# Optimization experiments

Hardware: AMD Instinct MI355X
Metric: run time of the kernel (lower is better)

Reference implementation:

```python
import jax, jax.numpy as jnp
import numpy as np


def setup_inputs() -> dict:
    key = jax.random.key(0)
    k0, k1, k2, k3, k4 = jax.random.split(key, 5)
    B, W, C, C2, D = 4, 64, 512, 512, 64  # D = C // k, k=8
    x = jax.random.normal(k0, (B, W, W, C), dtype=jnp.float32)
    input_h = jax.random.normal(k1, (B, W, W, C2), dtype=jnp.float32)
    f = jax.random.normal(k2, (1, 1, C2, D), dtype=jnp.float32) * 0.02
    g = jax.random.normal(k3, (1, 1, C, D), dtype=jnp.float32) * 0.02
    gamma = jax.random.uniform(k4, (1,), dtype=jnp.float32)
    return {"x": x, "input_h": input_h, "f": f, "g": g, "gamma": gamma}


def reference(x, input_h, f, g, gamma):
    # x: [B,W,W,C] NHWC, input_h: [B,W,W,C2], f: [1,1,C2,D], g: [1,1,C,D]
    B, W, _, C = x.shape
    C2 = input_h.shape[-1]
    N = W * W
    # 1x1 convs == per-pixel channel matmuls
    f_proj = jnp.einsum('bhwc,cd->bhwd', input_h, f[0, 0])  # [B,W,W,D]
    g_proj = jnp.einsum('bhwc,cd->bhwd', x, g[0, 0])        # [B,W,W,D]
    f_flat = f_proj.reshape(B, N, -1)
    g_flat = g_proj.reshape(B, N, -1)
    # unscaled attention scores over spatial positions
    s = jnp.einsum('bnd,bmd->bnm', g_flat, f_flat)          # [B,N,N]
    beta = jax.nn.softmax(s, axis=-1)
    h_flat = input_h.reshape(B, N, C2)
    o = jnp.einsum('bnm,bmc->bnc', beta, h_flat).reshape(B, W, W, C2)
    # mix_concat == 'mix': learned residual mix
    return gamma * o + x
```

## Files before the change

### kernel.cpp

```cpp
#include <hip/hip_runtime.h>
#include <hip/hip_bf16.h>
#include <cstdint>
#include <cstddef>


#define NPOS 4096
#define CCH  512
#define DQK  64
#define LSTR 72

typedef __attribute__((ext_vector_type(8)))  short s8v;
typedef __attribute__((ext_vector_type(4)))  short s4v;
typedef __attribute__((ext_vector_type(4)))  float f4v;

__device__ __forceinline__ float bf2f(unsigned short u) {
    unsigned int x = ((unsigned int)u) << 16;
    return __builtin_bit_cast(float, x);
}
__device__ __forceinline__ unsigned short f2bf(float f) {
    unsigned int u = __builtin_bit_cast(unsigned int, f);
    u += 0x7fffu + ((u >> 16) & 1u);
    return (unsigned short)(u >> 16);
}

__global__ __launch_bounds__(256) void wt_kernel(
    const float* __restrict__ f, const float* __restrict__ g,
    unsigned short* __restrict__ fT, unsigned short* __restrict__ gT)
{
    int gid = blockIdx.x * 256 + threadIdx.x;
    for (int e = 0; e < 4; ++e) {
        int i = e * 16384 + gid;
        int which = i >> 15;
        int j = i & 32767;
        int d = j >> 9, k = j & 511;
        const float* s = which ? g : f;
        unsigned short* dst = which ? gT : fT;
        dst[j] = f2bf(s[k * 64 + d]);
    }
}

__global__ __launch_bounds__(256) void vt_kernel(
    const float* __restrict__ ih, unsigned short* __restrict__ Vt)
{
    __shared__ unsigned short T[64 * 65];
    const int tid = threadIdx.x;
    const int bidx = blockIdx.x;
    const int bb = bidx >> 9;
    const int rem = bidx & 511;
    const int ct = rem >> 6;
    const int nt = rem & 63;

    for (int p = 0; p < 4; ++p) {
        int idx = p * 256 + tid;
        int r = idx >> 4, gg = idx & 15;
        f4v v = *(const f4v*)(ih + ((size_t)bb * NPOS + nt * 64 + r) * CCH + ct * 64 + gg * 4);
        for (int j = 0; j < 4; ++j) T[r * 65 + gg * 4 + j] = f2bf(v[j]);
    }
    __syncthreads();
    for (int p = 0; p < 2; ++p) {
        int idx = p * 256 + tid;
        int c = idx >> 3, ng = idx & 7;
        unsigned short tmp[8];
        for (int j = 0; j < 8; ++j) tmp[j] = T[(ng * 8 + j) * 65 + c];
        *(s8v*)(Vt + ((size_t)bb * CCH + ct * 64 + c) * NPOS + nt * 64 + ng * 8) = *(const s8v*)tmp;
    }
}

__global__ __launch_bounds__(256) void proj_kernel(
    const float* __restrict__ x,  const float* __restrict__ ih,
    const unsigned short* __restrict__ gT, const unsigned short* __restrict__ fT,
    unsigned short* __restrict__ Qg, unsigned short* __restrict__ Kf)
{
    __shared__ __align__(16) short Alds[128 * LSTR];
    __shared__ __align__(16) short Wlds[64 * LSTR];
    const int tid = threadIdx.x;
    const int wave = tid >> 6, lane = tid & 63;
    const int n15 = lane & 15, quad = lane >> 4;
    const int which = blockIdx.x >> 7;
    const int rb = (blockIdx.x & 127) * 128;
    const float* src = which ? ih : x;
    const unsigned short* wT  = which ? fT : gT;
    unsigned short* dst = which ? Kf : Qg;

    f4v acc[2][4];
    for (int i = 0; i < 2; ++i)
        for (int j = 0; j < 4; ++j)
            acc[i][j] = f4v{0.f, 0.f, 0.f, 0.f};

    for (int kc = 0; kc < 8; ++kc) {
        for (int p = 0; p < 8; ++p) {
            int idx = p * 256 + tid;
            int r = idx >> 4, gg = idx & 15;
            f4v v = *(const f4v*)(src + (size_t)(rb + r) * CCH + kc * 64 + gg * 4);
            s4v tv;
            for (int j = 0; j < 4; ++j) tv[j] = (short)f2bf(v[j]);
            *(s4v*)&Alds[r * LSTR + gg * 4] = tv;
        }
        for (int p = 0; p < 2; ++p) {
            int idx = p * 256 + tid;
            int c = idx >> 3, gg = idx & 7;
            *(s8v*)&Wlds[c * LSTR + gg * 8] =
                *(const s8v*)(wT + (size_t)c * CCH + kc * 64 + gg * 8);
        }
        __syncthreads();
        for (int kk = 0; kk < 2; ++kk) {
            s8v af0 = *(const s8v*)&Alds[(wave * 32 +      n15) * LSTR + kk * 32 + quad * 8];
            s8v af1 = *(const s8v*)&Alds[(wave * 32 + 16 + n15) * LSTR + kk * 32 + quad * 8];
            for (int ct = 0; ct < 4; ++ct) {
                s8v bf = *(const s8v*)&Wlds[(ct * 16 + n15) * LSTR + kk * 32 + quad * 8];
                acc[0][ct] = __builtin_amdgcn_mfma_f32_16x16x32_bf16(af0, bf, acc[0][ct], 0, 0, 0);
                acc[1][ct] = __builtin_amdgcn_mfma_f32_16x16x32_bf16(af1, bf, acc[1][ct], 0, 0, 0);
            }
        }
        __syncthreads();
    }
    for (int rt = 0; rt < 2; ++rt)
        for (int ct = 0; ct < 4; ++ct)
            for (int r = 0; r < 4; ++r) {
                int row = wave * 32 + rt * 16 + quad * 4 + r;
                int col = ct * 16 + n15;
                dst[(size_t)(rb + row) * DQK + col] = f2bf(acc[rt][ct][r]);
            }
}

__global__ __launch_bounds__(512) void flash_kernel(
    const unsigned short* __restrict__ Qg,
    const unsigned short* __restrict__ Kf,
    const unsigned short* __restrict__ Vt,
    const float* __restrict__ xin,
    const float* __restrict__ gptr,
    float* __restrict__ out)
{
    __shared__ __align__(16) short Klds[2 * 64 * LSTR];
    __shared__ __align__(16) short Plds[64 * LSTR];
    __shared__ float l_s[64];

    const int tid = threadIdx.x;
    const int wave = tid >> 6;
    const int lane = tid & 63;
    const int n15 = lane & 15, quad = lane >> 4;
    const int bid = blockIdx.x;
    const int xcd = bid & 7;
    const int b = xcd >> 1;
    const int qt = (xcd & 1) + ((bid >> 3) << 1);
    const int qbase = qt * 64;

    const float SOFT_M = 20.0f;
    float lpart = 0.0f;

    f4v acc[4][4];
    for (int i = 0; i < 4; ++i)
        for (int j = 0; j < 4; ++j)
            acc[i][j] = f4v{0.f, 0.f, 0.f, 0.f};

    const int ti = wave >> 1;
    const int mi0 = (wave & 1) * 2;
    s8v qf[2];
    {
        const unsigned short* qp =
            Qg + ((size_t)b * NPOS + qbase + ti * 16 + n15) * DQK + quad * 8;
        qf[0] = *(const s8v*)(qp);
        qf[1] = *(const s8v*)(qp + 32);
    }

    const int cb = wave * 64;
    const unsigned short* Vb = Vt + (size_t)b * CCH * NPOS;

    const int kr = tid >> 3, kg = tid & 7;
    const unsigned short* kbase_p = Kf + ((size_t)b * NPOS + kr) * DQK + kg * 8;
    s8v kreg = *(const s8v*)(kbase_p);

    for (int kb = 0; kb < NPOS / 64; ++kb) {
        const int m0 = kb * 64;
        *(s8v*)&Klds[(kb & 1) * 64 * LSTR + kr * LSTR + kg * 8] = kreg;
        if (kb + 1 < NPOS / 64)
            kreg = *(const s8v*)(kbase_p + (size_t)(m0 + 64) * DQK);
        s8v vf[4][2];
        for (int ct = 0; ct < 4; ++ct) {
            const unsigned short* vp =
                Vb + (size_t)(cb + ct * 16 + n15) * NPOS + m0 + quad * 8;
            vf[ct][0] = *(const s8v*)(vp);
            vf[ct][1] = *(const s8v*)(vp + 32);
        }
        __syncthreads();

        {
            const short* Kb = &Klds[(kb & 1) * 64 * LSTR];
            for (int mm = 0; mm < 2; ++mm) {
                const int mi = mi0 + mm;
                f4v s4 = f4v{0.f, 0.f, 0.f, 0.f};
                for (int ks = 0; ks < 2; ++ks) {
                    s8v kf = *(const s8v*)&Kb[(mi * 16 + n15) * LSTR + ks * 32 + quad * 8];
                    s4 = __builtin_amdgcn_mfma_f32_16x16x32_bf16(qf[ks], kf, s4, 0, 0, 0);
                }
                const int col = mi * 16 + n15;
                const int row0 = ti * 16 + quad * 4;
                for (int r = 0; r < 4; ++r)
                    Plds[(row0 + r) * LSTR + col] =
                        (short)f2bf(__expf(fminf(s4[r], 80.0f) - SOFT_M));
            }
        }
        __syncthreads();

        {
            const int r = tid >> 3, j8 = tid & 7;
            s8v p8 = *(const s8v*)&Plds[r * LSTR + j8 * 8];
            float ls = 0.f;
            for (int e = 0; e < 8; ++e) ls += bf2f((unsigned short)p8[e]);
            lpart += ls;
        }
        for (int kk = 0; kk < 2; ++kk) {
            s8v af[4];
            for (int q4 = 0; q4 < 4; ++q4)
                af[q4] = *(const s8v*)&Plds[(q4 * 16 + n15) * LSTR + kk * 32 + quad * 8];
            for (int q4 = 0; q4 < 4; ++q4)
                for (int ct = 0; ct < 4; ++ct)
                    acc[q4][ct] = __builtin_amdgcn_mfma_f32_16x16x32_bf16(
                        af[q4], vf[ct][kk], acc[q4][ct], 0, 0, 0);
        }
    }

    lpart += __shfl_xor(lpart, 1);
    lpart += __shfl_xor(lpart, 2);
    lpart += __shfl_xor(lpart, 4);
    if ((tid & 7) == 0) l_s[tid >> 3] = lpart;
    __syncthreads();

    const float gamma = gptr[0];
    for (int q4 = 0; q4 < 4; ++q4) {
        for (int r = 0; r < 4; ++r) {
            const int row = q4 * 16 + quad * 4 + r;
            const float sc = gamma / l_s[row];
            for (int ct = 0; ct < 4; ++ct) {
                const int col = cb + ct * 16 + n15;
                const size_t idx = ((size_t)b * NPOS + qbase + row) * CCH + col;
                out[idx] = acc[q4][ct][r] * sc + xin[idx];
            }
        }
    }
}

extern "C" void kernel_launch(void* const* d_in, const int* in_sizes, int n_in,
                              void* d_out, int out_size, void* d_ws, size_t ws_size,
                              hipStream_t stream)
{
    const float* x     = (const float*)d_in[0];
    const float* ih    = (const float*)d_in[1];
    const float* f     = (const float*)d_in[2];
    const float* g     = (const float*)d_in[3];
    const float* gamma = (const float*)d_in[4];
    float* out = (float*)d_out;

    char* ws = (char*)d_ws;
    unsigned short* fT = (unsigned short*)(ws + 0);
    unsigned short* gT = (unsigned short*)(ws + 65536);
    unsigned short* Qg = (unsigned short*)(ws + 131072);
    unsigned short* Kf = (unsigned short*)(ws + 2228224);
    unsigned short* Vt = (unsigned short*)(ws + 4325376);

    wt_kernel<<<64, 256, 0, stream>>>(f, g, fT, gT);
    vt_kernel<<<2048, 256, 0, stream>>>(ih, Vt);
    proj_kernel<<<256, 256, 0, stream>>>(x, ih, gT, fT, Qg, Kf);
    flash_kernel<<<256, 512, 0, stream>>>(Qg, Kf, Vt, x, gamma, out);
}
```

Before: 279.5 us.

## Split flash attention across channel halves and load K directly into registers

The flash kernel now runs 512 blocks of 256 threads. Each block covers half the output channels, and each wave computes the scores for its own 16 query rows. K is loaded straight from global memory into registers instead of being staged in LDS, and P is double-buffered, which removes one barrier per key tile. Row sums are accumulated in fp32 from the unrounded probabilities. The projection kernel also drops LDS and computes directly from global memory with one wave per 16 rows. The cost is that scores and exponentials are recomputed twice, once per channel half, and global K loads are redundant across waves.

```diff
diff --git a/kernel.cpp b/kernel.cpp
--- a/kernel.cpp
+++ b/kernel.cpp
@@ -10,7 +10,6 @@
 #define LSTR 72
 
 typedef __attribute__((ext_vector_type(8)))  short s8v;
-typedef __attribute__((ext_vector_type(4)))  short s4v;
 typedef __attribute__((ext_vector_type(4)))  float f4v;
 
 __device__ __forceinline__ float bf2f(unsigned short u) {
@@ -71,59 +70,41 @@
     const unsigned short* __restrict__ gT, const unsigned short* __restrict__ fT,
     unsigned short* __restrict__ Qg, unsigned short* __restrict__ Kf)
 {
-    __shared__ __align__(16) short Alds[128 * LSTR];
-    __shared__ __align__(16) short Wlds[64 * LSTR];
     const int tid = threadIdx.x;
     const int wave = tid >> 6, lane = tid & 63;
     const int n15 = lane & 15, quad = lane >> 4;
-    const int which = blockIdx.x >> 7;
-    const int rb = (blockIdx.x & 127) * 128;
+    const int which = blockIdx.x >> 8;
+    const int rbase = (blockIdx.x & 255) * 64 + wave * 16;
     const float* src = which ? ih : x;
     const unsigned short* wT  = which ? fT : gT;
     unsigned short* dst = which ? Kf : Qg;
 
-    f4v acc[2][4];
-    for (int i = 0; i < 2; ++i)
-        for (int j = 0; j < 4; ++j)
-            acc[i][j] = f4v{0.f, 0.f, 0.f, 0.f};
-
-    for (int kc = 0; kc < 8; ++kc) {
-        for (int p = 0; p < 8; ++p) {
-            int idx = p * 256 + tid;
-            int r = idx >> 4, gg = idx & 15;
-            f4v v = *(const f4v*)(src + (size_t)(rb + r) * CCH + kc * 64 + gg * 4);
-            s4v tv;
-            for (int j = 0; j < 4; ++j) tv[j] = (short)f2bf(v[j]);
-            *(s4v*)&Alds[r * LSTR + gg * 4] = tv;
-        }
-        for (int p = 0; p < 2; ++p) {
-            int idx = p * 256 + tid;
-            int c = idx >> 3, gg = idx & 7;
-            *(s8v*)&Wlds[c * LSTR + gg * 8] =
-                *(const s8v*)(wT + (size_t)c * CCH + kc * 64 + gg * 8);
-        }
-        __syncthreads();
-        for (int kk = 0; kk < 2; ++kk) {
-            s8v af0 = *(const s8v*)&Alds[(wave * 32 +      n15) * LSTR + kk * 32 + quad * 8];
-            s8v af1 = *(const s8v*)&Alds[(wave * 32 + 16 + n15) * LSTR + kk * 32 + quad * 8];
-            for (int ct = 0; ct < 4; ++ct) {
-                s8v bf = *(const s8v*)&Wlds[(ct * 16 + n15) * LSTR + kk * 32 + quad * 8];
-                acc[0][ct] = __builtin_amdgcn_mfma_f32_16x16x32_bf16(af0, bf, acc[0][ct], 0, 0, 0);
-                acc[1][ct] = __builtin_amdgcn_mfma_f32_16x16x32_bf16(af1, bf, acc[1][ct], 0, 0, 0);
-            }
-        }
-        __syncthreads();
-    }
-    for (int rt = 0; rt < 2; ++rt)
-        for (int ct = 0; ct < 4; ++ct)
-            for (int r = 0; r < 4; ++r) {
-                int row = wave * 32 + rt * 16 + quad * 4 + r;
-                int col = ct * 16 + n15;
-                dst[(size_t)(rb + row) * DQK + col] = f2bf(acc[rt][ct][r]);
-            }
-}
-
-__global__ __launch_bounds__(512) void flash_kernel(
+    f4v acc[4];
+    for (int ct = 0; ct < 4; ++ct) acc[ct] = f4v{0.f, 0.f, 0.f, 0.f};
+
+    const float* ap = src + (size_t)(rbase + n15) * CCH + quad * 8;
+    const unsigned short* bp = wT + (size_t)n15 * CCH + quad * 8;
+
+    for (int kc = 0; kc < 16; ++kc) {
+        f4v a0 = *(const f4v*)(ap + kc * 32);
+        f4v a1 = *(const f4v*)(ap + kc * 32 + 4);
+        s8v af;
+        for (int j = 0; j < 4; ++j) {
+            af[j]     = (short)f2bf(a0[j]);
+            af[4 + j] = (short)f2bf(a1[j]);
+        }
+        for (int ct = 0; ct < 4; ++ct) {
+            s8v bf = *(const s8v*)(bp + (size_t)(ct * 16) * CCH + kc * 32);
+            acc[ct] = __builtin_amdgcn_mfma_f32_16x16x32_bf16(af, bf, acc[ct], 0, 0, 0);
+        }
+    }
+    for (int ct = 0; ct < 4; ++ct)
+        for (int r = 0; r < 4; ++r)
+            dst[(size_t)(rbase + quad * 4 + r) * DQK + ct * 16 + n15] =
+                f2bf(acc[ct][r]);
+}
+
+__global__ __launch_bounds__(256) void flash_kernel(
     const unsigned short* __restrict__ Qg,
     const unsigned short* __restrict__ Kf,
     const unsigned short* __restrict__ Vt,
@@ -131,8 +112,7 @@
     const float* __restrict__ gptr,
     float* __restrict__ out)
 {
-    __shared__ __align__(16) short Klds[2 * 64 * LSTR];
-    __shared__ __align__(16) short Plds[64 * LSTR];
+    __shared__ __align__(16) short Plds[2][64 * LSTR];
     __shared__ float l_s[64];
 
     const int tid = threadIdx.x;
@@ -142,39 +122,35 @@
     const int bid = blockIdx.x;
     const int xcd = bid & 7;
     const int b = xcd >> 1;
-    const int qt = (xcd & 1) + ((bid >> 3) << 1);
+    const int idx2 = bid >> 3;
+    const int chalf = idx2 & 1;
+    const int qt = (xcd & 1) + ((idx2 >> 1) << 1);
     const int qbase = qt * 64;
+    const int cb = chalf * 256 + wave * 64;
 
     const float SOFT_M = 20.0f;
-    float lpart = 0.0f;
+    float lden[4] = {0.f, 0.f, 0.f, 0.f};
 
     f4v acc[4][4];
     for (int i = 0; i < 4; ++i)
         for (int j = 0; j < 4; ++j)
             acc[i][j] = f4v{0.f, 0.f, 0.f, 0.f};
 
-    const int ti = wave >> 1;
-    const int mi0 = (wave & 1) * 2;
     s8v qf[2];
     {
         const unsigned short* qp =
-            Qg + ((size_t)b * NPOS + qbase + ti * 16 + n15) * DQK + quad * 8;
+            Qg + ((size_t)b * NPOS + qbase + wave * 16 + n15) * DQK + quad * 8;
         qf[0] = *(const s8v*)(qp);
         qf[1] = *(const s8v*)(qp + 32);
     }
 
-    const int cb = wave * 64;
+    const unsigned short* Kb = Kf + (size_t)b * NPOS * DQK;
     const unsigned short* Vb = Vt + (size_t)b * CCH * NPOS;
-
-    const int kr = tid >> 3, kg = tid & 7;
-    const unsigned short* kbase_p = Kf + ((size_t)b * NPOS + kr) * DQK + kg * 8;
-    s8v kreg = *(const s8v*)(kbase_p);
 
     for (int kb = 0; kb < NPOS / 64; ++kb) {
         const int m0 = kb * 64;
-        *(s8v*)&Klds[(kb & 1) * 64 * LSTR + kr * LSTR + kg * 8] = kreg;
-        if (kb + 1 < NPOS / 64)
-            kreg = *(const s8v*)(kbase_p + (size_t)(m0 + 64) * DQK);
+        short* Pb = &Plds[kb & 1][0];
+
         s8v vf[4][2];
         for (int ct = 0; ct < 4; ++ct) {
             const unsigned short* vp =
@@ -182,37 +158,32 @@
             vf[ct][0] = *(const s8v*)(vp);
             vf[ct][1] = *(const s8v*)(vp + 32);
         }
+
+        s8v kf[4][2];
+        for (int mi = 0; mi < 4; ++mi) {
+            const unsigned short* kp =
+                Kb + (size_t)(m0 + mi * 16 + n15) * DQK + quad * 8;
+            kf[mi][0] = *(const s8v*)(kp);
+            kf[mi][1] = *(const s8v*)(kp + 32);
+        }
+        for (int mi = 0; mi < 4; ++mi) {
+            f4v s4 = f4v{0.f, 0.f, 0.f, 0.f};
+            s4 = __builtin_amdgcn_mfma_f32_16x16x32_bf16(qf[0], kf[mi][0], s4, 0, 0, 0);
+            s4 = __builtin_amdgcn_mfma_f32_16x16x32_bf16(qf[1], kf[mi][1], s4, 0, 0, 0);
+            const int col = mi * 16 + n15;
+            const int row0 = wave * 16 + quad * 4;
+            for (int r = 0; r < 4; ++r) {
+                float p = __expf(fminf(s4[r], 80.0f) - SOFT_M);
+                lden[r] += p;
+                Pb[(row0 + r) * LSTR + col] = (short)f2bf(p);
+            }
+        }
         __syncthreads();
 
-        {
-            const short* Kb = &Klds[(kb & 1) * 64 * LSTR];
-            for (int mm = 0; mm < 2; ++mm) {
-                const int mi = mi0 + mm;
-                f4v s4 = f4v{0.f, 0.f, 0.f, 0.f};
-                for (int ks = 0; ks < 2; ++ks) {
-                    s8v kf = *(const s8v*)&Kb[(mi * 16 + n15) * LSTR + ks * 32 + quad * 8];
-                    s4 = __builtin_amdgcn_mfma_f32_16x16x32_bf16(qf[ks], kf, s4, 0, 0, 0);
-                }
-                const int col = mi * 16 + n15;
-                const int row0 = ti * 16 + quad * 4;
-                for (int r = 0; r < 4; ++r)
-                    Plds[(row0 + r) * LSTR + col] =
-                        (short)f2bf(__expf(fminf(s4[r], 80.0f) - SOFT_M));
-            }
-        }
-        __syncthreads();
-
-        {
-            const int r = tid >> 3, j8 = tid & 7;
-            s8v p8 = *(const s8v*)&Plds[r * LSTR + j8 * 8];
-            float ls = 0.f;
-            for (int e = 0; e < 8; ++e) ls += bf2f((unsigned short)p8[e]);
-            lpart += ls;
-        }
         for (int kk = 0; kk < 2; ++kk) {
             s8v af[4];
             for (int q4 = 0; q4 < 4; ++q4)
-                af[q4] = *(const s8v*)&Plds[(q4 * 16 + n15) * LSTR + kk * 32 + quad * 8];
+                af[q4] = *(const s8v*)&Pb[(q4 * 16 + n15) * LSTR + kk * 32 + quad * 8];
             for (int q4 = 0; q4 < 4; ++q4)
                 for (int ct = 0; ct < 4; ++ct)
                     acc[q4][ct] = __builtin_amdgcn_mfma_f32_16x16x32_bf16(
@@ -220,10 +191,15 @@
         }
     }
 
-    lpart += __shfl_xor(lpart, 1);
-    lpart += __shfl_xor(lpart, 2);
-    lpart += __shfl_xor(lpart, 4);
-    if ((tid & 7) == 0) l_s[tid >> 3] = lpart;
+    for (int r = 0; r < 4; ++r) {
+        lden[r] += __shfl_xor(lden[r], 1);
+        lden[r] += __shfl_xor(lden[r], 2);
+        lden[r] += __shfl_xor(lden[r], 4);
+        lden[r] += __shfl_xor(lden[r], 8);
+    }
+    if (n15 == 0)
+        for (int r = 0; r < 4; ++r)
+            l_s[wave * 16 + quad * 4 + r] = lden[r];
     __syncthreads();
 
     const float gamma = gptr[0];
@@ -260,6 +236,6 @@
 
     wt_kernel<<<64, 256, 0, stream>>>(f, g, fT, gT);
     vt_kernel<<<2048, 256, 0, stream>>>(ih, Vt);
-    proj_kernel<<<256, 256, 0, stream>>>(x, ih, gT, fT, Qg, Kf);
-    flash_kernel<<<256, 512, 0, stream>>>(Qg, Kf, Vt, x, gamma, out);
-}
+    proj_kernel<<<512, 256, 0, stream>>>(x, ih, gT, fT, Qg, Kf);
+    flash_kernel<<<512, 256, 0, stream>>>(Qg, Kf, Vt, x, gamma, out);
+}
```

New measurement: 361.9 us. 29.5% more time.
